# Kernel optimization log

Hardware: AMD Instinct MI355X
Metric: run time of the kernel (lower is better)

The kernel has to match this reference:

```python
import jax, jax.numpy as jnp
import numpy as np

B, N, E, H = 4, 2048, 288, 8
D = E // H  # head_dim = 36


def setup_inputs() -> dict:
    key = jax.random.key(0)
    ks = jax.random.split(key, 8)
    s = 1.0 / np.sqrt(E)
    return {
        "query": jax.random.normal(ks[0], (B, N, E), jnp.float32),
        "key": jax.random.normal(ks[1], (B, N, E), jnp.float32),
        "value": jax.random.normal(ks[2], (B, N, E), jnp.float32),
        "Wq": jax.random.normal(ks[3], (E, E), jnp.float32) * s,
        "bq": jnp.zeros((E,), jnp.float32),
        "Wk": jax.random.normal(ks[4], (E, E), jnp.float32) * s,
        "bk": jnp.zeros((E,), jnp.float32),
        "Wv": jax.random.normal(ks[5], (E, E), jnp.float32) * s,
        "bv": jnp.zeros((E,), jnp.float32),
        "Wo": jax.random.normal(ks[6], (E, E), jnp.float32) * s,
        "bo": jnp.zeros((E,), jnp.float32),
    }


def reference(query, key, value, Wq, bq, Wk, bk, Wv, bv, Wo, bo):
    scaling = float(D) ** (-0.5)
    q = (query @ Wq + bq) * scaling            # (B, N, E), pre-scaled as in source
    k = key @ Wk + bk                          # (B, N, E)
    v = value @ Wv + bv                        # (B, N, E)
    # split heads: per-head slices along last dim == reshape to (B, N, H, D)
    qh = q.reshape(B, N, H, D)
    kh = k.reshape(B, N, H, D)
    vh = v.reshape(B, N, H, D)
    scores = jnp.einsum("bnhd,bmhd->bhnm", qh, kh)   # (B, H, N, N)
    attn = jax.nn.softmax(scores, axis=-1)
    out = jnp.einsum("bhnm,bmhd->bnhd", attn, vh)    # (B, N, H, D)
    out = out.reshape(B, N, E)                       # concat heads
    return out @ Wo + bo
```

## Files before the change

kernel.cpp:

```cpp
#include <hip/hip_runtime.h>

#define E 288
#define NSEQ 2048
#define BATCH 4
#define NH 8
#define HD 36
#define BH (BATCH * NH)
#define ROWS (BATCH * NSEQ)
#define BHN (BH * NSEQ)

typedef _Float16 half8_t __attribute__((ext_vector_type(8)));
typedef _Float16 half4_t __attribute__((ext_vector_type(4)));
typedef _Float16 half2_t __attribute__((ext_vector_type(2)));
typedef float f32x4 __attribute__((ext_vector_type(4)));
typedef int i32x4 __attribute__((ext_vector_type(4)));

__device__ __forceinline__ int sw64(int row, int col) {
  return (row << 6) + ((((col >> 3) ^ row) & 7) << 3) + (col & 7);
}

__device__ __forceinline__ int toff(int r, int k) {
  const int rp = r >> 1;
  const int g = (((r & 1) << 2) + (k >> 3)) ^ (rp & 7);
  return (rp << 6) + ((g & 7) << 3) + (k & 7);
}

__device__ __forceinline__ void gld16(const _Float16* g, _Float16* l) {
  __builtin_amdgcn_global_load_lds(
      (const __attribute__((address_space(1))) void*)g,
      (__attribute__((address_space(3))) void*)l, 16, 0, 0);
}

__device__ __forceinline__ float fexp2(float x) {
  return __builtin_amdgcn_exp2f(x);
}

__device__ __forceinline__ unsigned pack_h2(float a, float b) {
  union { half2_t h; unsigned u; } cv;
  cv.h[0] = (_Float16)a;
  cv.h[1] = (_Float16)b;
  return cv.u;
}

__device__ __forceinline__ void plswap16(unsigned& a, unsigned& b) {
  asm("v_permlane16_swap_b32 %0, %1" : "+v"(a), "+v"(b));
}
__device__ __forceinline__ void plswap32(unsigned& a, unsigned& b) {
  asm("v_permlane32_swap_b32 %0, %1" : "+v"(a), "+v"(b));
}

#define WBLK 1296
#define QZBLK 1024
#define VOBLK 256

__global__ __launch_bounds__(256) void prep_kernel(
    const float* __restrict__ Wq, const float* __restrict__ Wk,
    const float* __restrict__ Wv, const float* __restrict__ Wo,
    _Float16* __restrict__ wblk, _Float16* __restrict__ q16,
    _Float16* __restrict__ vblk) {
  const int bid = blockIdx.x;
  const int tid = threadIdx.x;
  if (bid < WBLK) {
    const int j = bid * 256 + tid;
    const int m = j / (E * E);
    const int rem = j - m * (E * E);
    const int k = rem / E, n = rem - k * E;
    const float* W = (m == 0) ? Wq : (m == 1) ? Wk : (m == 2) ? Wv : Wo;
    wblk[(size_t)((m * 3 + n / 96) * 9 + (k >> 5)) * 3072 +
         toff(n % 96, k & 31)] = (_Float16)W[(size_t)k * E + n];
  } else if (bid < WBLK + QZBLK) {
    const int j = (bid - WBLK) * 256 + tid;
    const int row = j >> 2, sub = j & 3;
    ((i32x4*)q16)[(size_t)row * 8 + 4 + sub] = (i32x4){0, 0, 0, 0};
  } else {
    const int j = (bid - WBLK - QZBLK) * 256 + tid;
    const int bh = j >> 11;
    const int rem = j & 2047;
    const int kt = rem >> 6, c = rem & 63;
    vblk[((size_t)bh * 32 + kt) * 3072 + sw64(36, c)] = (_Float16)1.0f;
  }
}

#define PM 128
#define PN 96

struct QKVArgs {
  const float* x[3];
  const float* bias[3];
  _Float16* out[3];
};

__global__ __launch_bounds__(256, 4) void proj_qkv_kernel(
    QKVArgs A, const _Float16* __restrict__ wblk) {
  __shared__ __align__(16) _Float16 abuf[2][4096];
  __shared__ __align__(16) _Float16 wbuf[2][3072];

  const int tid = threadIdx.x;
  const int lane = tid & 63, w = tid >> 6;
  const int quad = lane >> 4, l15 = lane & 15;
  const int mode = blockIdx.z;
  const int RB = blockIdx.x, CT = blockIdx.y;
  const float* __restrict__ x = A.x[mode];
  const _Float16* __restrict__ wb = wblk + (size_t)(mode * 3 + CT) * 9 * 3072;
  const int row0 = RB * PM;

  float4 apre[4];
  auto loadA = [&](int C) {
#pragma unroll
    for (int iu = 0; iu < 4; ++iu) {
      const int i = tid + 256 * iu, r = i >> 3, c4 = i & 7;
      apre[iu] = *(const float4*)&x[(size_t)(row0 + r) * E + C * 32 + c4 * 4];
    }
  };
  auto writeA = [&](_Float16* dst) {
#pragma unroll
    for (int iu = 0; iu < 4; ++iu) {
      const int i = tid + 256 * iu, r = i >> 3, c4 = i & 7;
      half4_t h = {(_Float16)apre[iu].x, (_Float16)apre[iu].y,
                   (_Float16)apre[iu].z, (_Float16)apre[iu].w};
      *(half4_t*)&dst[toff(r, c4 * 4)] = h;
    }
  };

  f32x4 acc[2][6];
#pragma unroll
  for (int t = 0; t < 2; ++t)
#pragma unroll
    for (int nt = 0; nt < 6; ++nt) acc[t][nt] = (f32x4){0.f, 0.f, 0.f, 0.f};

  loadA(0);
  writeA(abuf[0]);
  for (int seg = w; seg < 6; seg += 4)
    gld16(wb + seg * 512 + lane * 8, wbuf[0] + seg * 512);
  loadA(1);

  for (int C = 0; C < 9; ++C) {
    const int cur = C & 1;
    __syncthreads();
    if (C + 1 < 9) {
      for (int seg = w; seg < 6; seg += 4)
        gld16(wb + (C + 1) * 3072 + seg * 512 + lane * 8,
              wbuf[cur ^ 1] + seg * 512);
      writeA(abuf[cur ^ 1]);
      if (C + 2 < 9) loadA(C + 2);
    }
    half8_t ah[2];
#pragma unroll
    for (int t = 0; t < 2; ++t)
      ah[t] = *(const half8_t*)&abuf[cur][toff(w * 32 + t * 16 + l15, quad * 8)];
#pragma unroll
    for (int nt = 0; nt < 6; ++nt) {
      const half8_t bf = *(const half8_t*)&wbuf[cur][toff(nt * 16 + l15, quad * 8)];
#pragma unroll
      for (int t = 0; t < 2; ++t)
        acc[t][nt] = __builtin_amdgcn_mfma_f32_16x16x32_f16(ah[t], bf, acc[t][nt], 0, 0, 0);
    }
  }

  const float* __restrict__ bias = A.bias[mode];
  _Float16* __restrict__ outp = A.out[mode];
  const float scale = (mode == 0) ? 0.24044917348149868f : 1.0f;
  const int col0 = CT * PN;
#pragma unroll
  for (int nt = 0; nt < 6; ++nt) {
    const int col = col0 + nt * 16 + l15;
    const int h = col / 36, d = col - h * 36;
    const float bc = bias[col];
#pragma unroll
    for (int t = 0; t < 2; ++t) {
#pragma unroll
      for (int r = 0; r < 4; ++r) {
        const int row = row0 + w * 32 + t * 16 + quad * 4 + r;
        const int b = row >> 11, n = row & (NSEQ - 1);
        const int bh = b * NH + h;
        const _Float16 val = (_Float16)((acc[t][nt][r] + bc) * scale);
        if (mode == 0) {
          outp[((size_t)bh * NSEQ + n) * 64 + d] = val;
        } else {
          const int kt = n >> 6, c = n & 63;
          if (mode == 1) {
            outp[((size_t)bh * 32 + kt) * 4096 + sw64(c, d)] = val;
          } else {
            const int pc = ((c & 15) << 2) | (c >> 4);
            outp[((size_t)bh * 32 + kt) * 3072 + sw64(d, pc)] = val;
          }
        }
      }
    }
  }
}

#define QB 128
#define KT 64
#define SPLIT 2
#define NIT (32 / SPLIT)

__device__ __forceinline__ void stage_tile(const _Float16* kg, const _Float16* vg,
                                           _Float16* kb, _Float16* vb, int w,
                                           int lane) {
#pragma unroll
  for (int seg = w; seg < 8; seg += 4)
    gld16(kg + seg * 512 + lane * 8, kb + seg * 512);
  for (int seg = w; seg < 6; seg += 4)
    gld16(vg + seg * 512 + lane * 8, vb + seg * 512);
}

__global__ __launch_bounds__(256, 4) void attn_kernel(
    const _Float16* __restrict__ q16, const _Float16* __restrict__ kblk,
    const _Float16* __restrict__ vblk, _Float16* __restrict__ pacc16,
    float* __restrict__ psum) {
  __shared__ __align__(16) _Float16 kbuf[2][KT * 64];
  __shared__ __align__(16) _Float16 vbuf[2][48 * 64];

  const int tid = threadIdx.x;
  const int lane = tid & 63;
  const int w = tid >> 6;
  const int quad = lane >> 4;
  const int l15 = lane & 15;

  const int id = blockIdx.x;
  const int xcd = id & 7;
  const int qb = (id >> 3) & 15;
  const int g = id >> 7;
  const int bhc = g * 8 + xcd;
  const int bh = bhc >> 1;
  const int chunk = bhc & 1;
  const int q0 = qb * QB;

  const _Float16* qbase = q16 + ((size_t)bh * NSEQ + q0 + w * 32) * 64;
  half8_t qf[2][2];
#pragma unroll
  for (int t = 0; t < 2; ++t)
#pragma unroll
    for (int kc = 0; kc < 2; ++kc)
      qf[t][kc] = *(const half8_t*)&qbase[(t * 16 + l15) * 64 + kc * 32 + quad * 8];

  f32x4 oacc[2][3];
#pragma unroll
  for (int t = 0; t < 2; ++t)
#pragma unroll
    for (int nt = 0; nt < 3; ++nt) oacc[t][nt] = (f32x4){0.f, 0.f, 0.f, 0.f};

  const f32x4 zf = (f32x4){0.f, 0.f, 0.f, 0.f};

  const int t0 = chunk * NIT;
  const _Float16* kbase = kblk + ((size_t)bh * 32 + t0) * 4096;
  const _Float16* vbase = vblk + ((size_t)bh * 32 + t0) * 3072;

  stage_tile(kbase, vbase, kbuf[0], vbuf[0], w, lane);

  for (int it = 0; it < NIT; ++it) {
    const int cur = it & 1;
    __syncthreads();
    if (it + 1 < NIT)
      stage_tile(kbase + (it + 1) * 4096, vbase + (it + 1) * 3072,
                 kbuf[cur ^ 1], vbuf[cur ^ 1], w, lane);

    half8_t vf[2][3];
#pragma unroll
    for (int kc = 0; kc < 2; ++kc)
#pragma unroll
      for (int nt = 0; nt < 3; ++nt)
        vf[kc][nt] = *(const half8_t*)&vbuf[cur][sw64(nt * 16 + l15, kc * 32 + quad * 8)];

    unsigned pk[2][4][2];
#pragma unroll
    for (int a = 0; a < 2; ++a) {
      f32x4 sc[2][2];
      __builtin_amdgcn_s_setprio(1);
#pragma unroll
      for (int sp = 0; sp < 2; ++sp) {
        const int s = a * 2 + sp;
        const half8_t kf0 = *(const half8_t*)&kbuf[cur][sw64(s * 16 + l15, quad * 8)];
        const half8_t kf1 = *(const half8_t*)&kbuf[cur][sw64(s * 16 + l15, 32 + quad * 8)];
#pragma unroll
        for (int t = 0; t < 2; ++t) {
          f32x4 c0 = __builtin_amdgcn_mfma_f32_16x16x32_f16(
              kf0, qf[t][0], zf, 0, 0, 0);
          sc[t][sp] = __builtin_amdgcn_mfma_f32_16x16x32_f16(
              kf1, qf[t][1], c0, 0, 0, 0);
        }
      }
      __builtin_amdgcn_s_setprio(0);
#pragma unroll
      for (int t = 0; t < 2; ++t)
#pragma unroll
        for (int r = 0; r < 4; ++r) {
          const float p0 = fexp2(sc[t][0][r]);
          const float p1 = fexp2(sc[t][1][r]);
          pk[t][r][a] = pack_h2(p0, p1);
        }
    }

    half8_t pa[2][2];
#pragma unroll
    for (int t = 0; t < 2; ++t) {
      union { unsigned u[4]; half8_t h; } f0, f1;
#pragma unroll
      for (int v = 0; v < 4; ++v) {
        unsigned x = pk[t][v >> 1][v & 1];
        unsigned y = pk[t][(v >> 1) + 2][v & 1];
        plswap16(x, y);
        plswap32(x, y);
        f0.u[v] = x;
        f1.u[v] = y;
      }
      pa[t][0] = f0.h;
      pa[t][1] = f1.h;
    }

    __builtin_amdgcn_s_setprio(1);
#pragma unroll
    for (int kc = 0; kc < 2; ++kc)
#pragma unroll
      for (int nt = 0; nt < 3; ++nt) {
#pragma unroll
        for (int t = 0; t < 2; ++t)
          oacc[t][nt] = __builtin_amdgcn_mfma_f32_16x16x32_f16(pa[t][kc], vf[kc][nt], oacc[t][nt], 0, 0, 0);
      }
    __builtin_amdgcn_s_setprio(0);
  }

#pragma unroll
  for (int t = 0; t < 2; ++t) {
#pragma unroll
    for (int r = 0; r < 4; ++r) {
      const int row = q0 + w * 32 + t * 16 + quad * 4 + r;
      const size_t gr = (size_t)chunk * BHN + (size_t)bh * NSEQ + row;
      if (l15 == 4) psum[gr] = oacc[t][2][r];
#pragma unroll
      for (int nt = 0; nt < 3; ++nt) {
        const int col = nt * 16 + l15;
        if (col < HD) pacc16[gr * HD + col] = (_Float16)oacc[t][nt][r];
      }
    }
  }
}

__global__ __launch_bounds__(256) void combine_kernel(
    const _Float16* __restrict__ pacc16, const float* __restrict__ psum,
    _Float16* __restrict__ abh, _Float16* __restrict__ abl) {
  const int idx = blockIdx.x * 256 + threadIdx.x;
  if (idx >= BHN * 9) return;
  const int gr = idx / 9;
  const int d4 = idx - gr * 9;

  float a[4] = {0.f, 0.f, 0.f, 0.f};
  float s = 0.f;
#pragma unroll
  for (int c = 0; c < SPLIT; ++c) {
    const half4_t p = *(const half4_t*)&pacc16[((size_t)c * BHN + gr) * HD + d4 * 4];
#pragma unroll
    for (int j = 0; j < 4; ++j) a[j] += (float)p[j];
    s += psum[(size_t)c * BHN + gr];
  }
  const float inv = 1.0f / s;
  const int bh = gr >> 11;
  const int n = gr & (NSEQ - 1);
  const int b = bh >> 3, h = bh & 7;
  const int row = b * NSEQ + n;
  const int col = h * 36 + d4 * 4;

  half4_t hv, lv;
#pragma unroll
  for (int j = 0; j < 4; ++j) {
    const float val = a[j] * inv;
    const _Float16 hi = (_Float16)val;
    hv[j] = hi;
    lv[j] = (_Float16)(val - (float)hi);
  }
  const size_t o = (size_t)((row >> 6) * 9 + (col >> 5)) * 2048 + toff(row & 63, col & 31);
  *(half4_t*)&abh[o] = hv;
  *(half4_t*)&abl[o] = lv;
}

__global__ __launch_bounds__(256, 4) void proj_o_kernel(
    const _Float16* __restrict__ abh, const _Float16* __restrict__ abl,
    const _Float16* __restrict__ wblk_o, const float* __restrict__ bias,
    float* __restrict__ out) {
  __shared__ __align__(16) _Float16 hbuf[2][2048];
  __shared__ __align__(16) _Float16 lbuf[2][2048];
  __shared__ __align__(16) _Float16 wbuf[2][3072];

  const int tid = threadIdx.x;
  const int lane = tid & 63, w = tid >> 6;
  const int quad = lane >> 4, l15 = lane & 15;
  const int RB = blockIdx.x, CT = blockIdx.y;
  const _Float16* __restrict__ hblk = abh + (size_t)RB * 9 * 2048;
  const _Float16* __restrict__ lblk = abl + (size_t)RB * 9 * 2048;
  const _Float16* __restrict__ wb = wblk_o + (size_t)CT * 9 * 3072;

  f32x4 acc[6];
#pragma unroll
  for (int nt = 0; nt < 6; ++nt) acc[nt] = (f32x4){0.f, 0.f, 0.f, 0.f};

  gld16(hblk + w * 512 + lane * 8, hbuf[0] + w * 512);
  gld16(lblk + w * 512 + lane * 8, lbuf[0] + w * 512);
  for (int seg = w; seg < 6; seg += 4)
    gld16(wb + seg * 512 + lane * 8, wbuf[0] + seg * 512);

  for (int C = 0; C < 9; ++C) {
    const int cur = C & 1;
    __syncthreads();
    if (C + 1 < 9) {
      gld16(hblk + (C + 1) * 2048 + w * 512 + lane * 8, hbuf[cur ^ 1] + w * 512);
      gld16(lblk + (C + 1) * 2048 + w * 512 + lane * 8, lbuf[cur ^ 1] + w * 512);
      for (int seg = w; seg < 6; seg += 4)
        gld16(wb + (C + 1) * 3072 + seg * 512 + lane * 8, wbuf[cur ^ 1] + seg * 512);
    }
    const half8_t ah = *(const half8_t*)&hbuf[cur][toff(w * 16 + l15, quad * 8)];
    const half8_t al = *(const half8_t*)&lbuf[cur][toff(w * 16 + l15, quad * 8)];
#pragma unroll
    for (int nt = 0; nt < 6; ++nt) {
      const half8_t bf = *(const half8_t*)&wbuf[cur][toff(nt * 16 + l15, quad * 8)];
      acc[nt] = __builtin_amdgcn_mfma_f32_16x16x32_f16(ah, bf, acc[nt], 0, 0, 0);
      acc[nt] = __builtin_amdgcn_mfma_f32_16x16x32_f16(al, bf, acc[nt], 0, 0, 0);
    }
  }

#pragma unroll
  for (int nt = 0; nt < 6; ++nt) {
    const int col = CT * PN + nt * 16 + l15;
    const float bc = bias[col];
#pragma unroll
    for (int r = 0; r < 4; ++r) {
      const int row = RB * 64 + w * 16 + quad * 4 + r;
      out[(size_t)row * E + col] = acc[nt][r] + bc;
    }
  }
}

extern "C" void kernel_launch(void* const* d_in, const int* in_sizes, int n_in,
                              void* d_out, int out_size, void* d_ws,
                              size_t ws_size, hipStream_t stream) {
  const float* query = (const float*)d_in[0];
  const float* key_ = (const float*)d_in[1];
  const float* value = (const float*)d_in[2];
  const float* Wq = (const float*)d_in[3];
  const float* bq = (const float*)d_in[4];
  const float* Wk = (const float*)d_in[5];
  const float* bk = (const float*)d_in[6];
  const float* Wv = (const float*)d_in[7];
  const float* bv = (const float*)d_in[8];
  const float* Wo = (const float*)d_in[9];
  const float* bo = (const float*)d_in[10];
  float* out = (float*)d_out;

  _Float16* q16 = (_Float16*)d_ws;
  _Float16* kblk = q16 + (size_t)BH * NSEQ * 64;
  _Float16* vblk = kblk + (size_t)BH * 32 * 4096;
  _Float16* wblk = vblk + (size_t)BH * 32 * 3072;
  _Float16* abh = wblk + (size_t)4 * 3 * 9 * 3072;
  _Float16* abl = abh + (size_t)128 * 9 * 2048;
  _Float16* pacc16 = abl + (size_t)128 * 9 * 2048;
  float* psum = (float*)(pacc16 + (size_t)SPLIT * BHN * HD);

  prep_kernel<<<WBLK + QZBLK + VOBLK, 256, 0, stream>>>(Wq, Wk, Wv, Wo, wblk,
                                                        q16, vblk);

  QKVArgs qa;
  qa.x[0] = query; qa.x[1] = key_; qa.x[2] = value;
  qa.bias[0] = bq; qa.bias[1] = bk; qa.bias[2] = bv;
  qa.out[0] = q16; qa.out[1] = kblk; qa.out[2] = vblk;
  proj_qkv_kernel<<<dim3(ROWS / PM, E / PN, 3), 256, 0, stream>>>(qa, wblk);

  attn_kernel<<<dim3((NSEQ / QB) * BH * SPLIT), 256, 0, stream>>>(
      q16, kblk, vblk, pacc16, psum);

  combine_kernel<<<(BHN * 9) / 256, 256, 0, stream>>>(pacc16, psum, abh, abl);

  proj_o_kernel<<<dim3(ROWS / 64, E / PN), 256, 0, stream>>>(
      abh, abl, wblk + (size_t)3 * 3 * 9 * 3072, bo, out);
}
```

Measured before the change: 157.2 us.

## Software-pipeline QK of next tile with PV of previous tile using triple-buffered V

Restructures the attention inner loop so the QK^T and exp of tile p runs before the PV matmul of tile p-1. This lets the exp/pack work overlap with MFMA work across iterations. V shared buffers go from two to three so tile p-1's V stays valid while tile p+1 is being staged. Occupancy hint drops from 4 to 3 blocks per CU to make room for the extra LDS and the double set of P registers. The full unroll of the 16-iteration loop may increase code size and register pressure.

```diff
diff --git a/kernel.cpp b/kernel.cpp
--- a/kernel.cpp
+++ b/kernel.cpp
@@ -195,22 +195,12 @@
 #define SPLIT 2
 #define NIT (32 / SPLIT)
 
-__device__ __forceinline__ void stage_tile(const _Float16* kg, const _Float16* vg,
-                                           _Float16* kb, _Float16* vb, int w,
-                                           int lane) {
-#pragma unroll
-  for (int seg = w; seg < 8; seg += 4)
-    gld16(kg + seg * 512 + lane * 8, kb + seg * 512);
-  for (int seg = w; seg < 6; seg += 4)
-    gld16(vg + seg * 512 + lane * 8, vb + seg * 512);
-}
-
-__global__ __launch_bounds__(256, 4) void attn_kernel(
+__global__ __launch_bounds__(256, 3) void attn_kernel(
     const _Float16* __restrict__ q16, const _Float16* __restrict__ kblk,
     const _Float16* __restrict__ vblk, _Float16* __restrict__ pacc16,
     float* __restrict__ psum) {
   __shared__ __align__(16) _Float16 kbuf[2][KT * 64];
-  __shared__ __align__(16) _Float16 vbuf[2][48 * 64];
+  __shared__ __align__(16) _Float16 vbuf[3][48 * 64];
 
   const int tid = threadIdx.x;
   const int lane = tid & 63;
@@ -247,22 +237,26 @@
   const _Float16* kbase = kblk + ((size_t)bh * 32 + t0) * 4096;
   const _Float16* vbase = vblk + ((size_t)bh * 32 + t0) * 3072;
 
-  stage_tile(kbase, vbase, kbuf[0], vbuf[0], w, lane);
-
-  for (int it = 0; it < NIT; ++it) {
-    const int cur = it & 1;
+  auto stage_k = [&](int it) {
+#pragma unroll
+    for (int seg = w; seg < 8; seg += 4)
+      gld16(kbase + it * 4096 + seg * 512 + lane * 8,
+            kbuf[it & 1] + seg * 512);
+  };
+  auto stage_v = [&](int it) {
+#pragma unroll
+    for (int seg = w; seg < 6; seg += 4)
+      gld16(vbase + it * 3072 + seg * 512 + lane * 8,
+            vbuf[it % 3] + seg * 512);
+  };
+
+  auto qk_step = [&](int it, half8_t (&pa)[2][2]) {
     __syncthreads();
-    if (it + 1 < NIT)
-      stage_tile(kbase + (it + 1) * 4096, vbase + (it + 1) * 3072,
-                 kbuf[cur ^ 1], vbuf[cur ^ 1], w, lane);
-
-    half8_t vf[2][3];
-#pragma unroll
-    for (int kc = 0; kc < 2; ++kc)
-#pragma unroll
-      for (int nt = 0; nt < 3; ++nt)
-        vf[kc][nt] = *(const half8_t*)&vbuf[cur][sw64(nt * 16 + l15, kc * 32 + quad * 8)];
-
+    if (it + 1 < NIT) {
+      stage_k(it + 1);
+      stage_v(it + 1);
+    }
+    const _Float16* kb = kbuf[it & 1];
     unsigned pk[2][4][2];
 #pragma unroll
     for (int a = 0; a < 2; ++a) {
@@ -271,8 +265,8 @@
 #pragma unroll
       for (int sp = 0; sp < 2; ++sp) {
         const int s = a * 2 + sp;
-        const half8_t kf0 = *(const half8_t*)&kbuf[cur][sw64(s * 16 + l15, quad * 8)];
-        const half8_t kf1 = *(const half8_t*)&kbuf[cur][sw64(s * 16 + l15, 32 + quad * 8)];
+        const half8_t kf0 = *(const half8_t*)&kb[sw64(s * 16 + l15, quad * 8)];
+        const half8_t kf1 = *(const half8_t*)&kb[sw64(s * 16 + l15, 32 + quad * 8)];
 #pragma unroll
         for (int t = 0; t < 2; ++t) {
           f32x4 c0 = __builtin_amdgcn_mfma_f32_16x16x32_f16(
@@ -291,8 +285,6 @@
           pk[t][r][a] = pack_h2(p0, p1);
         }
     }
-
-    half8_t pa[2][2];
 #pragma unroll
     for (int t = 0; t < 2; ++t) {
       union { unsigned u[4]; half8_t h; } f0, f1;
@@ -308,18 +300,40 @@
       pa[t][0] = f0.h;
       pa[t][1] = f1.h;
     }
-
+  };
+
+  auto pv_step = [&](int it, const half8_t (&pa)[2][2]) {
+    const _Float16* vb = vbuf[it % 3];
     __builtin_amdgcn_s_setprio(1);
 #pragma unroll
-    for (int kc = 0; kc < 2; ++kc)
+    for (int kc = 0; kc < 2; ++kc) {
 #pragma unroll
       for (int nt = 0; nt < 3; ++nt) {
+        const half8_t vf = *(const half8_t*)&vb[sw64(nt * 16 + l15, kc * 32 + quad * 8)];
 #pragma unroll
         for (int t = 0; t < 2; ++t)
-          oacc[t][nt] = __builtin_amdgcn_mfma_f32_16x16x32_f16(pa[t][kc], vf[kc][nt], oacc[t][nt], 0, 0, 0);
+          oacc[t][nt] = __builtin_amdgcn_mfma_f32_16x16x32_f16(
+              pa[t][kc], vf, oacc[t][nt], 0, 0, 0);
       }
+    }
     __builtin_amdgcn_s_setprio(0);
-  }
+  };
+
+  half8_t paA[2][2], paB[2][2];
+  stage_k(0);
+  stage_v(0);
+  qk_step(0, paA);
+#pragma unroll
+  for (int p = 1; p < NIT; ++p) {
+    if (p & 1) {
+      qk_step(p, paB);
+      pv_step(p - 1, paA);
+    } else {
+      qk_step(p, paA);
+      pv_step(p - 1, paB);
+    }
+  }
+  pv_step(NIT - 1, paB);
 
 #pragma unroll
   for (int t = 0; t < 2; ++t) {
```

Result: no change. 158.2 us (+0.7%).

## Fuse split-combine and normalization into output projection, narrow column tiles

Applied to the files above, without the earlier changes.

Removes the separate combine kernel. The attention kernel now writes its partial outputs directly in row-major (row, E) layout with a per-row, per-head sum array. The output projection loads both split partials, sums them, scales by the reciprocal softmax sum, and splits the result into hi/lo fp16 while staging into shared memory. It also halves the column tile to 48, which doubles the grid so the extra per-block A-side work is spread across more blocks. This saves a launch and a round trip through global memory, at the cost of recomputing the combine once per column tile and more per-block VALU work.

```diff
diff --git a/kernel.cpp b/kernel.cpp
--- a/kernel.cpp
+++ b/kernel.cpp
@@ -208,7 +208,7 @@
 __global__ __launch_bounds__(256, 4) void attn_kernel(
     const _Float16* __restrict__ q16, const _Float16* __restrict__ kblk,
     const _Float16* __restrict__ vblk, _Float16* __restrict__ pacc16,
-    float* __restrict__ psum) {
+    float* __restrict__ psum_r) {
   __shared__ __align__(16) _Float16 kbuf[2][KT * 64];
   __shared__ __align__(16) _Float16 vbuf[2][48 * 64];
 
@@ -321,97 +321,104 @@
     __builtin_amdgcn_s_setprio(0);
   }
 
+  const int b = bh >> 3, h = bh & 7;
 #pragma unroll
   for (int t = 0; t < 2; ++t) {
 #pragma unroll
     for (int r = 0; r < 4; ++r) {
-      const int row = q0 + w * 32 + t * 16 + quad * 4 + r;
-      const size_t gr = (size_t)chunk * BHN + (size_t)bh * NSEQ + row;
-      if (l15 == 4) psum[gr] = oacc[t][2][r];
+      const int n = q0 + w * 32 + t * 16 + quad * 4 + r;
+      const size_t rowg = (size_t)b * NSEQ + n;
+      const size_t base = ((size_t)chunk * ROWS + rowg) * E + h * 36;
+      if (l15 == 4) psum_r[((size_t)chunk * ROWS + rowg) * 8 + h] = oacc[t][2][r];
 #pragma unroll
       for (int nt = 0; nt < 3; ++nt) {
         const int col = nt * 16 + l15;
-        if (col < HD) pacc16[gr * HD + col] = (_Float16)oacc[t][nt][r];
+        if (col < HD) pacc16[base + col] = (_Float16)oacc[t][nt][r];
       }
     }
   }
 }
 
-__global__ __launch_bounds__(256) void combine_kernel(
-    const _Float16* __restrict__ pacc16, const float* __restrict__ psum,
-    _Float16* __restrict__ abh, _Float16* __restrict__ abl) {
-  const int idx = blockIdx.x * 256 + threadIdx.x;
-  if (idx >= BHN * 9) return;
-  const int gr = idx / 9;
-  const int d4 = idx - gr * 9;
-
-  float a[4] = {0.f, 0.f, 0.f, 0.f};
-  float s = 0.f;
-#pragma unroll
-  for (int c = 0; c < SPLIT; ++c) {
-    const half4_t p = *(const half4_t*)&pacc16[((size_t)c * BHN + gr) * HD + d4 * 4];
-#pragma unroll
-    for (int j = 0; j < 4; ++j) a[j] += (float)p[j];
-    s += psum[(size_t)c * BHN + gr];
-  }
-  const float inv = 1.0f / s;
-  const int bh = gr >> 11;
-  const int n = gr & (NSEQ - 1);
-  const int b = bh >> 3, h = bh & 7;
-  const int row = b * NSEQ + n;
-  const int col = h * 36 + d4 * 4;
-
-  half4_t hv, lv;
-#pragma unroll
-  for (int j = 0; j < 4; ++j) {
-    const float val = a[j] * inv;
-    const _Float16 hi = (_Float16)val;
-    hv[j] = hi;
-    lv[j] = (_Float16)(val - (float)hi);
-  }
-  const size_t o = (size_t)((row >> 6) * 9 + (col >> 5)) * 2048 + toff(row & 63, col & 31);
-  *(half4_t*)&abh[o] = hv;
-  *(half4_t*)&abl[o] = lv;
-}
-
 __global__ __launch_bounds__(256, 4) void proj_o_kernel(
-    const _Float16* __restrict__ abh, const _Float16* __restrict__ abl,
+    const _Float16* __restrict__ pacc16, const float* __restrict__ psum_r,
     const _Float16* __restrict__ wblk_o, const float* __restrict__ bias,
     float* __restrict__ out) {
   __shared__ __align__(16) _Float16 hbuf[2][2048];
   __shared__ __align__(16) _Float16 lbuf[2][2048];
-  __shared__ __align__(16) _Float16 wbuf[2][3072];
+  __shared__ __align__(16) _Float16 wbuf[2][1536];
+  __shared__ float invt[512];
 
   const int tid = threadIdx.x;
   const int lane = tid & 63, w = tid >> 6;
   const int quad = lane >> 4, l15 = lane & 15;
   const int RB = blockIdx.x, CT = blockIdx.y;
-  const _Float16* __restrict__ hblk = abh + (size_t)RB * 9 * 2048;
-  const _Float16* __restrict__ lblk = abl + (size_t)RB * 9 * 2048;
-  const _Float16* __restrict__ wb = wblk_o + (size_t)CT * 9 * 3072;
-
-  f32x4 acc[6];
-#pragma unroll
-  for (int nt = 0; nt < 6; ++nt) acc[nt] = (f32x4){0.f, 0.f, 0.f, 0.f};
-
-  gld16(hblk + w * 512 + lane * 8, hbuf[0] + w * 512);
-  gld16(lblk + w * 512 + lane * 8, lbuf[0] + w * 512);
-  for (int seg = w; seg < 6; seg += 4)
+  const int row0 = RB * 64;
+  const _Float16* __restrict__ wb =
+      wblk_o + (size_t)(CT >> 1) * 9 * 3072 + (CT & 1) * 1536;
+
+#pragma unroll
+  for (int u = 0; u < 2; ++u) {
+    const int idx = tid + u * 256;
+    const int r = idx >> 3, hh = idx & 7;
+    const float s = psum_r[(size_t)(row0 + r) * 8 + hh] +
+                    psum_r[((size_t)ROWS + row0 + r) * 8 + hh];
+    invt[idx] = 1.0f / s;
+  }
+
+  const int arow = tid >> 2;
+  const int acol8 = (tid & 3) * 8;
+  half8_t ap0, ap1;
+  auto loadA = [&](int C) {
+    const size_t off = (size_t)(row0 + arow) * E + C * 32 + acol8;
+    ap0 = *(const half8_t*)&pacc16[off];
+    ap1 = *(const half8_t*)&pacc16[(size_t)ROWS * E + off];
+  };
+  auto writeA = [&](int C, _Float16* hd, _Float16* ld) {
+    const int colb = C * 32 + acol8;
+    const int h0 = colb / 36;
+    const int h1 = (colb + 7) / 36;
+    const float i0 = invt[(arow << 3) + h0];
+    const float i1 = invt[(arow << 3) + h1];
+    const int split = h1 * 36 - colb;
+    half8_t hv, lv;
+#pragma unroll
+    for (int j = 0; j < 8; ++j) {
+      const float inv = (j < split) ? i0 : i1;
+      const float a = (float)ap0[j] + (float)ap1[j];
+      const float val = a * inv;
+      const _Float16 hi = (_Float16)val;
+      hv[j] = hi;
+      lv[j] = (_Float16)(val - (float)hi);
+    }
+    *(half8_t*)&hd[toff(arow, acol8)] = hv;
+    *(half8_t*)&ld[toff(arow, acol8)] = lv;
+  };
+
+  f32x4 acc[3];
+#pragma unroll
+  for (int nt = 0; nt < 3; ++nt) acc[nt] = (f32x4){0.f, 0.f, 0.f, 0.f};
+
+  loadA(0);
+  __syncthreads();
+  writeA(0, hbuf[0], lbuf[0]);
+  for (int seg = w; seg < 3; seg += 4)
     gld16(wb + seg * 512 + lane * 8, wbuf[0] + seg * 512);
+  loadA(1);
 
   for (int C = 0; C < 9; ++C) {
     const int cur = C & 1;
     __syncthreads();
     if (C + 1 < 9) {
-      gld16(hblk + (C + 1) * 2048 + w * 512 + lane * 8, hbuf[cur ^ 1] + w * 512);
-      gld16(lblk + (C + 1) * 2048 + w * 512 + lane * 8, lbuf[cur ^ 1] + w * 512);
-      for (int seg = w; seg < 6; seg += 4)
-        gld16(wb + (C + 1) * 3072 + seg * 512 + lane * 8, wbuf[cur ^ 1] + seg * 512);
+      for (int seg = w; seg < 3; seg += 4)
+        gld16(wb + (C + 1) * 3072 + seg * 512 + lane * 8,
+              wbuf[cur ^ 1] + seg * 512);
+      writeA(C + 1, hbuf[cur ^ 1], lbuf[cur ^ 1]);
+      if (C + 2 < 9) loadA(C + 2);
     }
     const half8_t ah = *(const half8_t*)&hbuf[cur][toff(w * 16 + l15, quad * 8)];
     const half8_t al = *(const half8_t*)&lbuf[cur][toff(w * 16 + l15, quad * 8)];
 #pragma unroll
-    for (int nt = 0; nt < 6; ++nt) {
+    for (int nt = 0; nt < 3; ++nt) {
       const half8_t bf = *(const half8_t*)&wbuf[cur][toff(nt * 16 + l15, quad * 8)];
       acc[nt] = __builtin_amdgcn_mfma_f32_16x16x32_f16(ah, bf, acc[nt], 0, 0, 0);
       acc[nt] = __builtin_amdgcn_mfma_f32_16x16x32_f16(al, bf, acc[nt], 0, 0, 0);
@@ -419,12 +426,12 @@
   }
 
 #pragma unroll
-  for (int nt = 0; nt < 6; ++nt) {
-    const int col = CT * PN + nt * 16 + l15;
+  for (int nt = 0; nt < 3; ++nt) {
+    const int col = CT * 48 + nt * 16 + l15;
     const float bc = bias[col];
 #pragma unroll
     for (int r = 0; r < 4; ++r) {
-      const int row = RB * 64 + w * 16 + quad * 4 + r;
+      const int row = row0 + w * 16 + quad * 4 + r;
       out[(size_t)row * E + col] = acc[nt][r] + bc;
     }
   }
@@ -450,10 +457,8 @@
   _Float16* kblk = q16 + (size_t)BH * NSEQ * 64;
   _Float16* vblk = kblk + (size_t)BH * 32 * 4096;
   _Float16* wblk = vblk + (size_t)BH * 32 * 3072;
-  _Float16* abh = wblk + (size_t)4 * 3 * 9 * 3072;
-  _Float16* abl = abh + (size_t)128 * 9 * 2048;
-  _Float16* pacc16 = abl + (size_t)128 * 9 * 2048;
-  float* psum = (float*)(pacc16 + (size_t)SPLIT * BHN * HD);
+  _Float16* pacc16 = wblk + (size_t)4 * 3 * 9 * 3072;
+  float* psum_r = (float*)(pacc16 + (size_t)SPLIT * ROWS * E);
 
   prep_kernel<<<WBLK + QZBLK + VOBLK, 256, 0, stream>>>(Wq, Wk, Wv, Wo, wblk,
                                                         q16, vblk);
@@ -465,10 +470,8 @@
   proj_qkv_kernel<<<dim3(ROWS / PM, E / PN, 3), 256, 0, stream>>>(qa, wblk);
 
   attn_kernel<<<dim3((NSEQ / QB) * BH * SPLIT), 256, 0, stream>>>(
-      q16, kblk, vblk, pacc16, psum);
-
-  combine_kernel<<<(BHN * 9) / 256, 256, 0, stream>>>(pacc16, psum, abh, abl);
-
-  proj_o_kernel<<<dim3(ROWS / 64, E / PN), 256, 0, stream>>>(
-      abh, abl, wblk + (size_t)3 * 3 * 9 * 3072, bo, out);
-}
+      q16, kblk, vblk, pacc16, psum_r);
+
+  proj_o_kernel<<<dim3(ROWS / 64, E / 48), 256, 0, stream>>>(
+      pacc16, psum_r, wblk + (size_t)3 * 3 * 9 * 3072, bo, out);
+}
```

Result: no change. 157.1 us (-0.0%).
